# Kernel optimization log

Hardware: AMD Instinct MI355X
Metric: run time of the kernel (lower is better)

## Reference

```python
import jax, jax.numpy as jnp
import numpy as np

B, N = 2, 8192


def setup_inputs() -> dict:
    key = jax.random.key(0)
    ks = jax.random.split(key, 12)
    p = lambda k: jax.random.normal(k, (1, 1), jnp.float32) * 0.5
    return {
        "x": jax.random.normal(ks[0], (B, N), jnp.float32),
        "DSM": jax.random.uniform(ks[1], (N, N), jnp.float32),
        "w1": p(ks[2]), "b1": jnp.zeros((1,), jnp.float32),
        "lw1": p(ks[3]), "lb1": jnp.zeros((1,), jnp.float32),
        "lw2": p(ks[4]), "lb2": jnp.zeros((1,), jnp.float32),
        "w2": p(ks[5]), "b2": jnp.zeros((1,), jnp.float32),
        "w3": p(ks[6]), "b3": jnp.zeros((1,), jnp.float32),
        "wa": p(ks[7]), "ba": jnp.zeros((1,), jnp.float32),
        "wv": p(ks[8]), "bv": jnp.zeros((1,), jnp.float32),
    }


def _gcn_weighted(h, adj, w, b):
    # PyG GCNConv(normalize=True) on a complete graph whose edge weights are
    # adj[src, dst]; all self-loops already exist, so add_remaining_self_loops
    # is a no-op. deg[c] = sum over incoming edge weights (column sum),
    # norm[r,c] = deg[r]^-1/2 * adj[r,c] * deg[c]^-1/2, scatter-add at targets.
    deg = jnp.sum(adj, axis=0)                              # [N]
    dinv = jnp.where(deg > 0, jax.lax.rsqrt(deg), 0.0)
    anorm = dinv[:, None] * adj * dinv[None, :]             # [src, dst]
    hw = h * w[0, 0]                                        # Linear(1,1,bias=False)
    out = jnp.einsum('rc,brd->bcd', anorm, hw)              # [B,N,1]
    return out + b


def _gcn_uniform(h, w, b):
    # edge_weight=None on the complete graph: deg = N everywhere, every
    # normalized edge weight = 1/N -> output at each node is the node-mean.
    m = jnp.mean(h * w[0, 0], axis=-2, keepdims=True)       # [B,1,1]
    return jnp.broadcast_to(m, h.shape) + b


def reference(x, DSM, w1, b1, lw1, lb1, lw2, lb2, w2, b2, w3, b3, wa, ba, wv, bv):
    h = x[:, :, None]                                       # [B,N,1]
    h = jax.nn.relu(_gcn_weighted(h, DSM, w1, b1))
    h = jax.nn.relu(h * lw1[0, 0] + lb1)
    h = jax.nn.relu(h * lw2[0, 0] + lb2)
    h = jax.nn.relu(_gcn_uniform(h, w2, b2))
    h = jax.nn.relu(_gcn_uniform(h, w3, b3))
    action_prob = jax.nn.softmax(h * wa[0, 0] + ba, axis=-1)  # [B,N,1]
    u = jnp.max(h, axis=0, keepdims=True)                   # MaxAggregation dim=0
    v = jnp.max(u, axis=-2, keepdims=True)                  # MaxAggregation dim=-2
    state_values = v * wv[0, 0] + bv                        # [1,1,1]
    return action_prob, state_values
```

## Files before the change

kernel.cpp:

```cpp
#include <hip/hip_runtime.h>
#include <math.h>

#define N 8192
#define NV4 (N / 4)
#define RPB 64
#define NBY (N / RPB)
#define GRID_X 8
#define THREADS 256

#define DEGP_OFF  0
#define TPART_OFF (NBY * N)
#define HPART_OFF (TPART_OFF + NBY * 2 * N)

__global__ void k_colsum(const float* __restrict__ dsm, float* __restrict__ degp) {
    int chunk = (blockIdx.x + blockIdx.y) & (GRID_X - 1);
    int c4 = chunk * THREADS + threadIdx.x;
    int r0 = blockIdx.y * RPB;
    const float4* p = (const float4*)dsm;
    float4 acc = {0.f, 0.f, 0.f, 0.f};
#pragma unroll 16
    for (int i = 0; i < RPB; ++i) {
        float4 v = p[(size_t)(r0 + i) * NV4 + c4];
        acc.x += v.x; acc.y += v.y; acc.z += v.z; acc.w += v.w;
    }
    ((float4*)(degp + (size_t)blockIdx.y * N))[c4] = acc;
}

__global__ void k_matvec(const float* __restrict__ dsm, const float* __restrict__ degp,
                         const float* __restrict__ x, float* __restrict__ tpart) {
    __shared__ float sred[4 * RPB];
    __shared__ float sg0[RPB];
    __shared__ float sg1[RPB];
    int r0 = blockIdx.y * RPB;

    {
        int rl = threadIdx.x & 63;
        int q  = threadIdx.x >> 6;
        const float* dp = degp + r0 + rl;
        float s = 0.f;
#pragma unroll 8
        for (int j = 0; j < 32; ++j) s += dp[(size_t)(q * 32 + j) * N];
        sred[q * RPB + rl] = s;
    }
    __syncthreads();
    if (threadIdx.x < RPB) {
        int r = threadIdx.x;
        float d = sred[r] + sred[RPB + r] + sred[2 * RPB + r] + sred[3 * RPB + r];
        float di = d > 0.f ? rsqrtf(d) : 0.f;
        sg0[r] = di * x[r0 + r];
        sg1[r] = di * x[N + r0 + r];
    }
    __syncthreads();

    int chunk = (blockIdx.x + blockIdx.y) & (GRID_X - 1);
    int c4 = chunk * THREADS + threadIdx.x;
    const float4* p = (const float4*)dsm;
    float4 a0 = {0.f, 0.f, 0.f, 0.f};
    float4 a1 = {0.f, 0.f, 0.f, 0.f};
#pragma unroll 16
    for (int i = 0; i < RPB; ++i) {
        float4 v = p[(size_t)(r0 + i) * NV4 + c4];
        float g0 = sg0[i], g1 = sg1[i];
        a0.x += v.x * g0; a0.y += v.y * g0; a0.z += v.z * g0; a0.w += v.w * g0;
        a1.x += v.x * g1; a1.y += v.y * g1; a1.z += v.z * g1; a1.w += v.w * g1;
    }
    ((float4*)(tpart + ((size_t)blockIdx.y * 2 + 0) * N))[c4] = a0;
    ((float4*)(tpart + ((size_t)blockIdx.y * 2 + 1) * N))[c4] = a1;
}

__global__ void k_head(const float* __restrict__ degp, const float* __restrict__ tpart,
                       const float* __restrict__ w1, const float* __restrict__ b1,
                       const float* __restrict__ lw1, const float* __restrict__ lb1,
                       const float* __restrict__ lw2, const float* __restrict__ lb2,
                       float* __restrict__ hpart, float* __restrict__ out) {
    __shared__ float swred[8];
    int c = blockIdx.x * THREADS + threadIdx.x;

    float d = 0.f, t0 = 0.f, t1 = 0.f;
#pragma unroll 8
    for (int by = 0; by < NBY; ++by) {
        d  += degp[(size_t)by * N + c];
        t0 += tpart[((size_t)by * 2 + 0) * N + c];
        t1 += tpart[((size_t)by * 2 + 1) * N + c];
    }
    float di = d > 0.f ? rsqrtf(d) : 0.f;

    float W1 = w1[0], B1 = b1[0];
    float LW1 = lw1[0], LB1 = lb1[0];
    float LW2 = lw2[0], LB2 = lb2[0];
    float h0 = fmaxf(W1 * di * t0 + B1, 0.f);
    h0 = fmaxf(h0 * LW1 + LB1, 0.f);
    h0 = fmaxf(h0 * LW2 + LB2, 0.f);
    float h1 = fmaxf(W1 * di * t1 + B1, 0.f);
    h1 = fmaxf(h1 * LW1 + LB1, 0.f);
    h1 = fmaxf(h1 * LW2 + LB2, 0.f);

    out[c] = 1.0f;
    out[N + c] = 1.0f;

    float v0 = h0, v1 = h1;
    for (int off = 32; off > 0; off >>= 1) {
        v0 += __shfl_down(v0, off);
        v1 += __shfl_down(v1, off);
    }
    int wave = threadIdx.x >> 6;
    if ((threadIdx.x & 63) == 0) { swred[wave] = v0; swred[4 + wave] = v1; }
    __syncthreads();
    if (threadIdx.x == 0) {
        hpart[blockIdx.x * 2 + 0] = swred[0] + swred[1] + swred[2] + swred[3];
        hpart[blockIdx.x * 2 + 1] = swred[4] + swred[5] + swred[6] + swred[7];
    }
}

__global__ void k_out(const float* __restrict__ hpart,
                      const float* __restrict__ w2, const float* __restrict__ b2,
                      const float* __restrict__ w3, const float* __restrict__ b3,
                      const float* __restrict__ wv, const float* __restrict__ bv,
                      float* __restrict__ out) {
    int tid = threadIdx.x;
    float s0 = tid < 32 ? hpart[tid * 2 + 0] : 0.f;
    float s1 = tid < 32 ? hpart[tid * 2 + 1] : 0.f;
    for (int off = 16; off > 0; off >>= 1) {
        s0 += __shfl_down(s0, off);
        s1 += __shfl_down(s1, off);
    }
    if (tid == 0) {
        float vmax = -INFINITY;
        float m0 = s0 * (1.0f / (float)N);
        float m1 = s1 * (1.0f / (float)N);
        float a = fmaxf(m0 * w2[0] + b2[0], 0.f);
        a = fmaxf(a * w3[0] + b3[0], 0.f);
        float b = fmaxf(m1 * w2[0] + b2[0], 0.f);
        b = fmaxf(b * w3[0] + b3[0], 0.f);
        vmax = fmaxf(a, b);
        out[2 * N] = vmax * wv[0] + bv[0];
    }
}

extern "C" void kernel_launch(void* const* d_in, const int* in_sizes, int n_in,
                              void* d_out, int out_size, void* d_ws, size_t ws_size,
                              hipStream_t stream) {
    const float* x   = (const float*)d_in[0];
    const float* dsm = (const float*)d_in[1];
    const float* w1  = (const float*)d_in[2];
    const float* b1  = (const float*)d_in[3];
    const float* lw1 = (const float*)d_in[4];
    const float* lb1 = (const float*)d_in[5];
    const float* lw2 = (const float*)d_in[6];
    const float* lb2 = (const float*)d_in[7];
    const float* w2  = (const float*)d_in[8];
    const float* b2  = (const float*)d_in[9];
    const float* w3  = (const float*)d_in[10];
    const float* b3  = (const float*)d_in[11];
    const float* wv  = (const float*)d_in[14];
    const float* bv  = (const float*)d_in[15];

    float* ws    = (float*)d_ws;
    float* degp  = ws + DEGP_OFF;
    float* tpart = ws + TPART_OFF;
    float* hpart = ws + HPART_OFF;

    dim3 big(GRID_X, NBY);
    k_colsum<<<big, THREADS, 0, stream>>>(dsm, degp);
    k_matvec<<<big, THREADS, 0, stream>>>(dsm, degp, x, tpart);
    k_head<<<N / THREADS, THREADS, 0, stream>>>(degp, tpart, w1, b1, lw1, lb1,
                                                lw2, lb2, hpart, (float*)d_out);
    k_out<<<1, 64, 0, stream>>>(hpart, w2, b2, w3, b3, wv, bv, (float*)d_out);
}
```

Before: 438.9 us.

## Fuse colsum and matvec into cooperative kernel with register and reverse-order reuse

Merges the degree column-sum and the normalized matvec into one cooperative kernel separated by a grid-wide sync. Each thread keeps its first rows of the matrix tile in registers and traverses the remaining rows in reverse during the second pass, so recently loaded lines are more likely still cached. The inverse-degree vector is written once so the head kernel no longer re-reduces degree partials. This relies on all blocks being co-resident and adds grid-sync cost and register pressure.

```diff
diff --git a/kernel.cpp b/kernel.cpp
--- a/kernel.cpp
+++ b/kernel.cpp
@@ -1,5 +1,8 @@
 #include <hip/hip_runtime.h>
+#include <hip/hip_cooperative_groups.h>
 #include <math.h>
+
+namespace cg = cooperative_groups;
 
 #define N 8192
 #define NV4 (N / 4)
@@ -7,31 +10,42 @@
 #define NBY (N / RPB)
 #define GRID_X 8
 #define THREADS 256
+#define CR 8
 
 #define DEGP_OFF  0
 #define TPART_OFF (NBY * N)
-#define HPART_OFF (TPART_OFF + NBY * 2 * N)
+#define DINV_OFF  (TPART_OFF + NBY * 2 * N)
+#define HPART_OFF (DINV_OFF + N)
 
-__global__ void k_colsum(const float* __restrict__ dsm, float* __restrict__ degp) {
+__global__ __launch_bounds__(THREADS, 4)
+void k_fused(const float* __restrict__ dsm, float* __restrict__ degp,
+             const float* __restrict__ x, float* __restrict__ dinvg,
+             float* __restrict__ tpart) {
+    __shared__ float sred[4 * RPB];
+    __shared__ float sg0[RPB];
+    __shared__ float sg1[RPB];
+
     int chunk = (blockIdx.x + blockIdx.y) & (GRID_X - 1);
     int c4 = chunk * THREADS + threadIdx.x;
     int r0 = blockIdx.y * RPB;
-    const float4* p = (const float4*)dsm;
+    const float4* p = (const float4*)dsm + (size_t)r0 * NV4 + c4;
+
+    float4 cache[CR];
     float4 acc = {0.f, 0.f, 0.f, 0.f};
-#pragma unroll 16
-    for (int i = 0; i < RPB; ++i) {
-        float4 v = p[(size_t)(r0 + i) * NV4 + c4];
+#pragma unroll
+    for (int i = 0; i < CR; ++i) {
+        float4 v = p[(size_t)i * NV4];
+        cache[i] = v;
+        acc.x += v.x; acc.y += v.y; acc.z += v.z; acc.w += v.w;
+    }
+#pragma unroll 8
+    for (int i = CR; i < RPB; ++i) {
+        float4 v = p[(size_t)i * NV4];
         acc.x += v.x; acc.y += v.y; acc.z += v.z; acc.w += v.w;
     }
     ((float4*)(degp + (size_t)blockIdx.y * N))[c4] = acc;
-}
 
-__global__ void k_matvec(const float* __restrict__ dsm, const float* __restrict__ degp,
-                         const float* __restrict__ x, float* __restrict__ tpart) {
-    __shared__ float sred[4 * RPB];
-    __shared__ float sg0[RPB];
-    __shared__ float sg1[RPB];
-    int r0 = blockIdx.y * RPB;
+    cg::this_grid().sync();
 
     {
         int rl = threadIdx.x & 63;
@@ -49,17 +63,22 @@
         float di = d > 0.f ? rsqrtf(d) : 0.f;
         sg0[r] = di * x[r0 + r];
         sg1[r] = di * x[N + r0 + r];
+        if (blockIdx.x == 0) dinvg[r0 + r] = di;
     }
     __syncthreads();
 
-    int chunk = (blockIdx.x + blockIdx.y) & (GRID_X - 1);
-    int c4 = chunk * THREADS + threadIdx.x;
-    const float4* p = (const float4*)dsm;
     float4 a0 = {0.f, 0.f, 0.f, 0.f};
     float4 a1 = {0.f, 0.f, 0.f, 0.f};
-#pragma unroll 16
-    for (int i = 0; i < RPB; ++i) {
-        float4 v = p[(size_t)(r0 + i) * NV4 + c4];
+#pragma unroll 8
+    for (int i = RPB - 1; i >= CR; --i) {
+        float4 v = p[(size_t)i * NV4];
+        float g0 = sg0[i], g1 = sg1[i];
+        a0.x += v.x * g0; a0.y += v.y * g0; a0.z += v.z * g0; a0.w += v.w * g0;
+        a1.x += v.x * g1; a1.y += v.y * g1; a1.z += v.z * g1; a1.w += v.w * g1;
+    }
+#pragma unroll
+    for (int i = 0; i < CR; ++i) {
+        float4 v = cache[i];
         float g0 = sg0[i], g1 = sg1[i];
         a0.x += v.x * g0; a0.y += v.y * g0; a0.z += v.z * g0; a0.w += v.w * g0;
         a1.x += v.x * g1; a1.y += v.y * g1; a1.z += v.z * g1; a1.w += v.w * g1;
@@ -68,7 +87,7 @@
     ((float4*)(tpart + ((size_t)blockIdx.y * 2 + 1) * N))[c4] = a1;
 }
 
-__global__ void k_head(const float* __restrict__ degp, const float* __restrict__ tpart,
+__global__ void k_head(const float* __restrict__ dinvg, const float* __restrict__ tpart,
                        const float* __restrict__ w1, const float* __restrict__ b1,
                        const float* __restrict__ lw1, const float* __restrict__ lb1,
                        const float* __restrict__ lw2, const float* __restrict__ lb2,
@@ -76,14 +95,13 @@
     __shared__ float swred[8];
     int c = blockIdx.x * THREADS + threadIdx.x;
 
-    float d = 0.f, t0 = 0.f, t1 = 0.f;
+    float t0 = 0.f, t1 = 0.f;
 #pragma unroll 8
     for (int by = 0; by < NBY; ++by) {
-        d  += degp[(size_t)by * N + c];
         t0 += tpart[((size_t)by * 2 + 0) * N + c];
         t1 += tpart[((size_t)by * 2 + 1) * N + c];
     }
-    float di = d > 0.f ? rsqrtf(d) : 0.f;
+    float di = dinvg[c];
 
     float W1 = w1[0], B1 = b1[0];
     float LW1 = lw1[0], LB1 = lb1[0];
@@ -125,14 +143,13 @@
         s1 += __shfl_down(s1, off);
     }
     if (tid == 0) {
-        float vmax = -INFINITY;
         float m0 = s0 * (1.0f / (float)N);
         float m1 = s1 * (1.0f / (float)N);
         float a = fmaxf(m0 * w2[0] + b2[0], 0.f);
         a = fmaxf(a * w3[0] + b3[0], 0.f);
         float b = fmaxf(m1 * w2[0] + b2[0], 0.f);
         b = fmaxf(b * w3[0] + b3[0], 0.f);
-        vmax = fmaxf(a, b);
+        float vmax = fmaxf(a, b);
         out[2 * N] = vmax * wv[0] + bv[0];
     }
 }
@@ -158,12 +175,13 @@
     float* ws    = (float*)d_ws;
     float* degp  = ws + DEGP_OFF;
     float* tpart = ws + TPART_OFF;
+    float* dinvg = ws + DINV_OFF;
     float* hpart = ws + HPART_OFF;
 
-    dim3 big(GRID_X, NBY);
-    k_colsum<<<big, THREADS, 0, stream>>>(dsm, degp);
-    k_matvec<<<big, THREADS, 0, stream>>>(dsm, degp, x, tpart);
-    k_head<<<N / THREADS, THREADS, 0, stream>>>(degp, tpart, w1, b1, lw1, lb1,
+    void* kargs[] = {(void*)&dsm, (void*)&degp, (void*)&x, (void*)&dinvg, (void*)&tpart};
+    hipLaunchCooperativeKernel((const void*)k_fused, dim3(GRID_X, NBY), dim3(THREADS),
+                               kargs, 0, stream);
+    k_head<<<N / THREADS, THREADS, 0, stream>>>(dinvg, tpart, w1, b1, lw1, lb1,
                                                 lw2, lb2, hpart, (float*)d_out);
     k_out<<<1, 64, 0, stream>>>(hpart, w2, b2, w3, b3, wv, bv, (float*)d_out);
 }
```

Measured after the change: 587.1 us. 33.8% more time.

## Hoist degree normalization into separate kernel, halve rows per block, nontemporal stores

Applied to the files above, without the earlier changes.

Adds a k_dinv kernel that computes the inverse-sqrt degree and the scaled inputs g0/g1 once per column. Previously every matvec block recomputed them from the partial column sums, and k_head summed the degree partials again. RPB is halved to 32, which doubles the grid and gives more parallelism. The cost is twice as many partial rows for k_head to reduce and more workspace traffic. Partial results are written with nontemporal stores so they do not pollute cache, and an extra kernel launch is added.

```diff
diff --git a/kernel.cpp b/kernel.cpp
--- a/kernel.cpp
+++ b/kernel.cpp
@@ -3,72 +3,80 @@
 
 #define N 8192
 #define NV4 (N / 4)
-#define RPB 64
+#define RPB 32
 #define NBY (N / RPB)
 #define GRID_X 8
 #define THREADS 256
 
+typedef float f4 __attribute__((ext_vector_type(4)));
+
 #define DEGP_OFF  0
 #define TPART_OFF (NBY * N)
-#define HPART_OFF (TPART_OFF + NBY * 2 * N)
+#define DINV_OFF  (TPART_OFF + NBY * 2 * N)
+#define G0_OFF    (DINV_OFF + N)
+#define G1_OFF    (G0_OFF + N)
+#define HPART_OFF (G1_OFF + N)
 
 __global__ void k_colsum(const float* __restrict__ dsm, float* __restrict__ degp) {
     int chunk = (blockIdx.x + blockIdx.y) & (GRID_X - 1);
     int c4 = chunk * THREADS + threadIdx.x;
     int r0 = blockIdx.y * RPB;
-    const float4* p = (const float4*)dsm;
-    float4 acc = {0.f, 0.f, 0.f, 0.f};
-#pragma unroll 16
-    for (int i = 0; i < RPB; ++i) {
-        float4 v = p[(size_t)(r0 + i) * NV4 + c4];
-        acc.x += v.x; acc.y += v.y; acc.z += v.z; acc.w += v.w;
-    }
-    ((float4*)(degp + (size_t)blockIdx.y * N))[c4] = acc;
+    const f4* p = (const f4*)dsm + (size_t)r0 * NV4 + c4;
+    f4 acc = 0.f;
+#pragma unroll 8
+    for (int i = 0; i < RPB; ++i) acc += p[(size_t)i * NV4];
+    __builtin_nontemporal_store(acc, (f4*)(degp + (size_t)blockIdx.y * N) + c4);
 }
 
-__global__ void k_matvec(const float* __restrict__ dsm, const float* __restrict__ degp,
-                         const float* __restrict__ x, float* __restrict__ tpart) {
-    __shared__ float sred[4 * RPB];
+__global__ void k_dinv(const float* __restrict__ degp, const float* __restrict__ x,
+                       float* __restrict__ dinvg, float* __restrict__ g0,
+                       float* __restrict__ g1) {
+    __shared__ float sred[4][64];
+    int c0 = blockIdx.x * 64;
+    int cl = threadIdx.x & 63;
+    int q  = threadIdx.x >> 6;
+    const float* dp = degp + c0 + cl;
+    float s = 0.f;
+#pragma unroll 8
+    for (int j = 0; j < NBY / 4; ++j) s += dp[(size_t)(q * (NBY / 4) + j) * N];
+    sred[q][cl] = s;
+    __syncthreads();
+    if (threadIdx.x < 64) {
+        int c = c0 + threadIdx.x;
+        float d = sred[0][threadIdx.x] + sred[1][threadIdx.x] +
+                  sred[2][threadIdx.x] + sred[3][threadIdx.x];
+        float di = d > 0.f ? rsqrtf(d) : 0.f;
+        dinvg[c] = di;
+        g0[c] = di * x[c];
+        g1[c] = di * x[N + c];
+    }
+}
+
+__global__ void k_matvec(const float* __restrict__ dsm, const float* __restrict__ g0,
+                         const float* __restrict__ g1, float* __restrict__ tpart) {
     __shared__ float sg0[RPB];
     __shared__ float sg1[RPB];
     int r0 = blockIdx.y * RPB;
-
-    {
-        int rl = threadIdx.x & 63;
-        int q  = threadIdx.x >> 6;
-        const float* dp = degp + r0 + rl;
-        float s = 0.f;
-#pragma unroll 8
-        for (int j = 0; j < 32; ++j) s += dp[(size_t)(q * 32 + j) * N];
-        sred[q * RPB + rl] = s;
+    if (threadIdx.x < RPB) {
+        sg0[threadIdx.x] = g0[r0 + threadIdx.x];
+        sg1[threadIdx.x] = g1[r0 + threadIdx.x];
     }
     __syncthreads();
-    if (threadIdx.x < RPB) {
-        int r = threadIdx.x;
-        float d = sred[r] + sred[RPB + r] + sred[2 * RPB + r] + sred[3 * RPB + r];
-        float di = d > 0.f ? rsqrtf(d) : 0.f;
-        sg0[r] = di * x[r0 + r];
-        sg1[r] = di * x[N + r0 + r];
-    }
-    __syncthreads();
-
     int chunk = (blockIdx.x + blockIdx.y) & (GRID_X - 1);
     int c4 = chunk * THREADS + threadIdx.x;
-    const float4* p = (const float4*)dsm;
-    float4 a0 = {0.f, 0.f, 0.f, 0.f};
-    float4 a1 = {0.f, 0.f, 0.f, 0.f};
-#pragma unroll 16
+    const f4* p = (const f4*)dsm + (size_t)r0 * NV4 + c4;
+    f4 a0 = 0.f, a1 = 0.f;
+#pragma unroll 8
     for (int i = 0; i < RPB; ++i) {
-        float4 v = p[(size_t)(r0 + i) * NV4 + c4];
-        float g0 = sg0[i], g1 = sg1[i];
-        a0.x += v.x * g0; a0.y += v.y * g0; a0.z += v.z * g0; a0.w += v.w * g0;
-        a1.x += v.x * g1; a1.y += v.y * g1; a1.z += v.z * g1; a1.w += v.w * g1;
+        f4 v = p[(size_t)i * NV4];
+        a0 += v * sg0[i];
+        a1 += v * sg1[i];
     }
-    ((float4*)(tpart + ((size_t)blockIdx.y * 2 + 0) * N))[c4] = a0;
-    ((float4*)(tpart + ((size_t)blockIdx.y * 2 + 1) * N))[c4] = a1;
+    __builtin_nontemporal_store(a0, (f4*)(tpart + ((size_t)blockIdx.y * 2 + 0) * N) + c4);
+    __builtin_nontemporal_store(a1, (f4*)(tpart + ((size_t)blockIdx.y * 2 + 1) * N) + c4);
 }
 
-__global__ void k_head(const float* __restrict__ degp, const float* __restrict__ tpart,
+__global__ void k_head(const float* __restrict__ dinvg, const float* __restrict__ tpart,
                        const float* __restrict__ w1, const float* __restrict__ b1,
                        const float* __restrict__ lw1, const float* __restrict__ lb1,
                        const float* __restrict__ lw2, const float* __restrict__ lb2,
@@ -76,14 +84,13 @@
     __shared__ float swred[8];
     int c = blockIdx.x * THREADS + threadIdx.x;
 
-    float d = 0.f, t0 = 0.f, t1 = 0.f;
+    float t0 = 0.f, t1 = 0.f;
 #pragma unroll 8
     for (int by = 0; by < NBY; ++by) {
-        d  += degp[(size_t)by * N + c];
         t0 += tpart[((size_t)by * 2 + 0) * N + c];
         t1 += tpart[((size_t)by * 2 + 1) * N + c];
     }
-    float di = d > 0.f ? rsqrtf(d) : 0.f;
+    float di = dinvg[c];
 
     float W1 = w1[0], B1 = b1[0];
     float LW1 = lw1[0], LB1 = lb1[0];
@@ -125,14 +132,13 @@
         s1 += __shfl_down(s1, off);
     }
     if (tid == 0) {
-        float vmax = -INFINITY;
         float m0 = s0 * (1.0f / (float)N);
         float m1 = s1 * (1.0f / (float)N);
         float a = fmaxf(m0 * w2[0] + b2[0], 0.f);
         a = fmaxf(a * w3[0] + b3[0], 0.f);
         float b = fmaxf(m1 * w2[0] + b2[0], 0.f);
         b = fmaxf(b * w3[0] + b3[0], 0.f);
-        vmax = fmaxf(a, b);
+        float vmax = fmaxf(a, b);
         out[2 * N] = vmax * wv[0] + bv[0];
     }
 }
@@ -158,12 +164,16 @@
     float* ws    = (float*)d_ws;
     float* degp  = ws + DEGP_OFF;
     float* tpart = ws + TPART_OFF;
+    float* dinvg = ws + DINV_OFF;
+    float* g0    = ws + G0_OFF;
+    float* g1    = ws + G1_OFF;
     float* hpart = ws + HPART_OFF;
 
     dim3 big(GRID_X, NBY);
     k_colsum<<<big, THREADS, 0, stream>>>(dsm, degp);
-    k_matvec<<<big, THREADS, 0, stream>>>(dsm, degp, x, tpart);
-    k_head<<<N / THREADS, THREADS, 0, stream>>>(degp, tpart, w1, b1, lw1, lb1,
+    k_dinv<<<N / 64, THREADS, 0, stream>>>(degp, x, dinvg, g0, g1);
+    k_matvec<<<big, THREADS, 0, stream>>>(dsm, g0, g1, tpart);
+    k_head<<<N / THREADS, THREADS, 0, stream>>>(dinvg, tpart, w1, b1, lw1, lb1,
                                                 lw2, lb2, hpart, (float*)d_out);
     k_out<<<1, 64, 0, stream>>>(hpart, w2, b2, w3, b3, wv, bv, (float*)d_out);
 }
```

New measurement: 470.8 us. +7.3%, slower.
